# Optimization experiments

Measured on AMD Instinct MI355X. Metric: run time of the kernel, lower is better.

Reference implementation:

```python
import jax, jax.numpy as jnp
import numpy as np

NUM_EXPERTS = 64
TOP_K = 8
TEMPERATURE = 1.0


def setup_inputs() -> dict:
    key = jax.random.key(0)
    k1, k2 = jax.random.split(key)
    B, D, E = 32768, 2048, NUM_EXPERTS
    r = jax.random.normal(k1, (B, D), dtype=jnp.float32)
    W = jax.random.normal(k2, (E, D), dtype=jnp.float32) * (1.0 / np.sqrt(D))
    b = jnp.zeros((E,), dtype=jnp.float32)
    return {"r": r, "W": W, "b": b}


def reference(r, W, b):
    # logits: (B, E) = r @ W^T + b, then temperature scaling
    logits = (jnp.einsum('bd,ed->be', r, W) + b) / TEMPERATURE
    weights_soft = jax.nn.softmax(logits, axis=-1)
    if TOP_K is not None and TOP_K < NUM_EXPERTS:
        topk_vals, topk_idx = jax.lax.top_k(weights_soft, TOP_K)
        mask = jnp.zeros_like(weights_soft)
        mask = jax.vmap(lambda m, i: m.at[i].set(1.0))(mask, topk_idx)
        weights_hard = weights_soft * mask
        weights_hard = weights_hard / (weights_hard.sum(axis=-1, keepdims=True) + 1e-9)
    else:
        weights_hard = weights_soft
    return (weights_hard, weights_soft)
```

## Files before the change

kernel.cpp:

```cpp
#include <hip/hip_runtime.h>
#include <hip/hip_bf16.h>
#include <stdint.h>


#define D_DIM 2048
#define E_DIM 64
#define B_DIM 32768
#define TOPK 8

typedef __bf16 bf16x8 __attribute__((ext_vector_type(8)));
typedef float f32x4 __attribute__((ext_vector_type(4)));

__global__ __launch_bounds__(256) void w_split3(const float* __restrict__ W,
                                                __bf16* __restrict__ W1,
                                                __bf16* __restrict__ W2,
                                                __bf16* __restrict__ W3) {
    int i = (blockIdx.x * 256 + threadIdx.x) * 8;
    bf16x8 o1, o2, o3;
    #pragma unroll
    for (int j = 0; j < 8; ++j) {
        float x  = W[i + j];
        __bf16 h1 = (__bf16)x;
        float r1 = x - (float)h1;
        __bf16 h2 = (__bf16)r1;
        float r2 = r1 - (float)h2;
        o1[j] = h1; o2[j] = h2; o3[j] = (__bf16)r2;
    }
    *(bf16x8*)(W1 + i) = o1;
    *(bf16x8*)(W2 + i) = o2;
    *(bf16x8*)(W3 + i) = o3;
}

__device__ __forceinline__ void gload_lds16(const void* g, void* s) {
    __builtin_amdgcn_global_load_lds(
        (const __attribute__((address_space(1))) unsigned int*)g,
        (__attribute__((address_space(3))) unsigned int*)s,
        16, 0, 0);
}

__global__ __launch_bounds__(256) void moe_gate(const float* __restrict__ r,
                                                const __bf16* __restrict__ W1,
                                                const __bf16* __restrict__ W2,
                                                const __bf16* __restrict__ W3,
                                                const float* __restrict__ bias,
                                                float* __restrict__ out) {
    __shared__ __bf16 bstage[2][3][E_DIM * 32];
    __shared__ float  lg[64][E_DIM + 1];

    const int t    = threadIdx.x;
    const int wv   = t >> 6;
    const int lane = t & 63;
    const int lrow = lane & 15;
    const int quad = lane >> 4;
    const int row0 = blockIdx.x * 64;

    const int se  = t >> 2;
    const int skc = t & 3;
    const size_t sgo = (size_t)se * D_DIM + skc * 8;

    const float* ra = r + (size_t)(row0 + wv * 16 + lrow) * D_DIM + quad * 8;

    f32x4 accM[4] = {};
    f32x4 accD[4] = {};
    f32x4 accL[4] = {};

    gload_lds16(W1 + sgo, &bstage[0][0][t * 8]);
    gload_lds16(W2 + sgo, &bstage[0][1][t * 8]);
    gload_lds16(W3 + sgo, &bstage[0][2][t * 8]);
    float4 a0 = *(const float4*)(ra);
    float4 a1 = *(const float4*)(ra + 4);

    for (int ks = 0; ks < D_DIM / 32; ++ks) {
        __syncthreads();
        const int kn = ks + 1;
        if (kn < D_DIM / 32) {
            const size_t go = sgo + (size_t)kn * 32;
            gload_lds16(W1 + go, &bstage[kn & 1][0][t * 8]);
            gload_lds16(W2 + go, &bstage[kn & 1][1][t * 8]);
            gload_lds16(W3 + go, &bstage[kn & 1][2][t * 8]);
        }

        float av[8] = {a0.x, a0.y, a0.z, a0.w, a1.x, a1.y, a1.z, a1.w};
        if (kn < D_DIM / 32) {
            a0 = *(const float4*)(ra + kn * 32);
            a1 = *(const float4*)(ra + kn * 32 + 4);
        }
        bf16x8 A1, A2, A3;
        #pragma unroll
        for (int j = 0; j < 8; ++j) {
            float x  = av[j];
            __bf16 h1 = (__bf16)x;
            float r1 = x - (float)h1;
            __bf16 h2 = (__bf16)r1;
            float r2 = r1 - (float)h2;
            A1[j] = h1; A2[j] = h2; A3[j] = (__bf16)r2;
        }

        const __bf16* bb = &bstage[ks & 1][0][0];
        const int fo = (quad * 8) + lrow * 32;
        bf16x8 B[3][4];
        #pragma unroll
        for (int s = 0; s < 3; ++s)
            #pragma unroll
            for (int n = 0; n < 4; ++n)
                B[s][n] = *(const bf16x8*)(bb + (size_t)s * E_DIM * 32 + n * 16 * 32 + fo);

        #pragma unroll
        for (int n = 0; n < 4; ++n) {
            accM[n] = __builtin_amdgcn_mfma_f32_16x16x32_bf16(A1, B[0][n], accM[n], 0, 0, 0);
            accD[n] = __builtin_amdgcn_mfma_f32_16x16x32_bf16(A1, B[1][n], accD[n], 0, 0, 0);
            accD[n] = __builtin_amdgcn_mfma_f32_16x16x32_bf16(A2, B[0][n], accD[n], 0, 0, 0);
            accL[n] = __builtin_amdgcn_mfma_f32_16x16x32_bf16(A1, B[2][n], accL[n], 0, 0, 0);
            accL[n] = __builtin_amdgcn_mfma_f32_16x16x32_bf16(A2, B[1][n], accL[n], 0, 0, 0);
            accL[n] = __builtin_amdgcn_mfma_f32_16x16x32_bf16(A3, B[0][n], accL[n], 0, 0, 0);
        }
    }

    #pragma unroll
    for (int n = 0; n < 4; ++n) {
        int col = n * 16 + lrow;
        float bb = bias[col];
        #pragma unroll
        for (int i = 0; i < 4; ++i) {
            lg[wv * 16 + quad * 4 + i][col] = (accM[n][i] + (accD[n][i] + accL[n][i])) + bb;
        }
    }
    __syncthreads();

    for (int rr = wv; rr < 64; rr += 4) {
        float logit = lg[rr][lane];
        float mx = logit;
        #pragma unroll
        for (int s = 32; s >= 1; s >>= 1) mx = fmaxf(mx, __shfl_xor(mx, s));
        float ex = expf(logit - mx);
        float sm = ex;
        #pragma unroll
        for (int s = 32; s >= 1; s >>= 1) sm += __shfl_xor(sm, s);
        float soft = ex / sm;

        bool  sel    = false;
        float topsum = 0.0f;
        #pragma unroll
        for (int it = 0; it < TOPK; ++it) {
            float cand = sel ? -1.0f : soft;
            float cm = cand;
            #pragma unroll
            for (int s = 32; s >= 1; s >>= 1) cm = fmaxf(cm, __shfl_xor(cm, s));
            unsigned long long ball = __ballot(cand == cm);
            int leader = __ffsll(ball) - 1;
            if (lane == leader) sel = true;
            topsum += cm;
        }
        float hard = sel ? soft / (topsum + 1e-9f) : 0.0f;

        size_t orow = (size_t)(row0 + rr) * E_DIM + lane;
        out[orow] = hard;
        out[(size_t)B_DIM * E_DIM + orow] = soft;
    }
}

extern "C" void kernel_launch(void* const* d_in, const int* in_sizes, int n_in,
                              void* d_out, int out_size, void* d_ws, size_t ws_size,
                              hipStream_t stream) {
    const float* r = (const float*)d_in[0];
    const float* W = (const float*)d_in[1];
    const float* b = (const float*)d_in[2];
    float* out = (float*)d_out;
    __bf16* W1 = (__bf16*)d_ws;
    __bf16* W2 = W1 + (size_t)E_DIM * D_DIM;
    __bf16* W3 = W2 + (size_t)E_DIM * D_DIM;

    w_split3<<<64, 256, 0, stream>>>(W, W1, W2, W3);
    moe_gate<<<512, 256, 0, stream>>>(r, W1, W2, W3, b, out);
}
```

Baseline: 433.0 us.

## Split K dimension across two wave groups and pack W chunks contiguously

Each block now runs 512 threads: two halves of four waves each take half of the D dimension for the same 64 rows, and their partial logits are summed through shared memory before the softmax/top-k stage. The weight prep kernel writes the three bf16 splits into a K-chunk-interleaved layout, so each stage load reads one contiguous 12 KB chunk. The shared staging buffer is reused for the logits tile. The aim is more waves in flight per CU to hide r-load latency, at the cost of an extra reduction pass and more barriers.

```diff
diff --git a/kernel.cpp b/kernel.cpp
--- a/kernel.cpp
+++ b/kernel.cpp
@@ -11,24 +11,25 @@
 typedef __bf16 bf16x8 __attribute__((ext_vector_type(8)));
 typedef float f32x4 __attribute__((ext_vector_type(4)));
 
-__global__ __launch_bounds__(256) void w_split3(const float* __restrict__ W,
-                                                __bf16* __restrict__ W1,
-                                                __bf16* __restrict__ W2,
-                                                __bf16* __restrict__ W3) {
-    int i = (blockIdx.x * 256 + threadIdx.x) * 8;
+__global__ __launch_bounds__(256) void w_prep(const float* __restrict__ W,
+                                              __bf16* __restrict__ P) {
+    const int K = blockIdx.x;
+    const int u = threadIdx.x;
+    const float* src = W + (size_t)(u >> 2) * D_DIM + K * 32 + (u & 3) * 8;
+    __bf16* dst = P + (size_t)K * 6144 + u * 8;
     bf16x8 o1, o2, o3;
     #pragma unroll
     for (int j = 0; j < 8; ++j) {
-        float x  = W[i + j];
+        float x  = src[j];
         __bf16 h1 = (__bf16)x;
         float r1 = x - (float)h1;
         __bf16 h2 = (__bf16)r1;
         float r2 = r1 - (float)h2;
         o1[j] = h1; o2[j] = h2; o3[j] = (__bf16)r2;
     }
-    *(bf16x8*)(W1 + i) = o1;
-    *(bf16x8*)(W2 + i) = o2;
-    *(bf16x8*)(W3 + i) = o3;
+    *(bf16x8*)(dst)        = o1;
+    *(bf16x8*)(dst + 2048) = o2;
+    *(bf16x8*)(dst + 4096) = o3;
 }
 
 __device__ __forceinline__ void gload_lds16(const void* g, void* s) {
@@ -38,50 +39,51 @@
         16, 0, 0);
 }
 
-__global__ __launch_bounds__(256) void moe_gate(const float* __restrict__ r,
-                                                const __bf16* __restrict__ W1,
-                                                const __bf16* __restrict__ W2,
-                                                const __bf16* __restrict__ W3,
-                                                const float* __restrict__ bias,
-                                                float* __restrict__ out) {
-    __shared__ __bf16 bstage[2][3][E_DIM * 32];
-    __shared__ float  lg[64][E_DIM + 1];
+__global__ __launch_bounds__(512, 4) void moe_gate(const float* __restrict__ r,
+                                                   const __bf16* __restrict__ P,
+                                                   const float* __restrict__ bias,
+                                                   float* __restrict__ out) {
+    __shared__ __align__(16) char smem[2 * 2 * 3 * 2048 * 2];
+
+    __bf16 (*bstage)[2][3][2048] = reinterpret_cast<__bf16 (*)[2][3][2048]>(smem);
+    float  (*lg)[E_DIM + 1]      = reinterpret_cast<float (*)[E_DIM + 1]>(smem);
 
     const int t    = threadIdx.x;
     const int wv   = t >> 6;
     const int lane = t & 63;
     const int lrow = lane & 15;
     const int quad = lane >> 4;
+    const int h    = wv >> 2;
+    const int wq   = wv & 3;
+    const int tl   = t & 255;
     const int row0 = blockIdx.x * 64;
 
-    const int se  = t >> 2;
-    const int skc = t & 3;
-    const size_t sgo = (size_t)se * D_DIM + skc * 8;
+    const __bf16* Pb = P + (size_t)h * 32 * 6144 + tl * 8;
 
-    const float* ra = r + (size_t)(row0 + wv * 16 + lrow) * D_DIM + quad * 8;
+    const float* ra = r + (size_t)(row0 + wq * 16 + lrow) * D_DIM + h * 1024 + quad * 8;
 
     f32x4 accM[4] = {};
     f32x4 accD[4] = {};
     f32x4 accL[4] = {};
 
-    gload_lds16(W1 + sgo, &bstage[0][0][t * 8]);
-    gload_lds16(W2 + sgo, &bstage[0][1][t * 8]);
-    gload_lds16(W3 + sgo, &bstage[0][2][t * 8]);
+    #pragma unroll
+    for (int s = 0; s < 3; ++s)
+        gload_lds16(Pb + s * 2048, &bstage[h][0][s][tl * 8]);
     float4 a0 = *(const float4*)(ra);
     float4 a1 = *(const float4*)(ra + 4);
 
-    for (int ks = 0; ks < D_DIM / 32; ++ks) {
+    for (int ks = 0; ks < 32; ++ks) {
         __syncthreads();
         const int kn = ks + 1;
-        if (kn < D_DIM / 32) {
-            const size_t go = sgo + (size_t)kn * 32;
-            gload_lds16(W1 + go, &bstage[kn & 1][0][t * 8]);
-            gload_lds16(W2 + go, &bstage[kn & 1][1][t * 8]);
-            gload_lds16(W3 + go, &bstage[kn & 1][2][t * 8]);
+        if (kn < 32) {
+            #pragma unroll
+            for (int s = 0; s < 3; ++s)
+                gload_lds16(Pb + (size_t)kn * 6144 + s * 2048,
+                            &bstage[h][kn & 1][s][tl * 8]);
         }
 
         float av[8] = {a0.x, a0.y, a0.z, a0.w, a1.x, a1.y, a1.z, a1.w};
-        if (kn < D_DIM / 32) {
+        if (kn < 32) {
             a0 = *(const float4*)(ra + kn * 32);
             a1 = *(const float4*)(ra + kn * 32 + 4);
         }
@@ -96,14 +98,14 @@
             A1[j] = h1; A2[j] = h2; A3[j] = (__bf16)r2;
         }
 
-        const __bf16* bb = &bstage[ks & 1][0][0];
-        const int fo = (quad * 8) + lrow * 32;
+        const __bf16* bb = &bstage[h][ks & 1][0][0];
+        const int fo = quad * 8 + lrow * 32;
         bf16x8 B[3][4];
         #pragma unroll
         for (int s = 0; s < 3; ++s)
             #pragma unroll
             for (int n = 0; n < 4; ++n)
-                B[s][n] = *(const bf16x8*)(bb + (size_t)s * E_DIM * 32 + n * 16 * 32 + fo);
+                B[s][n] = *(const bf16x8*)(bb + (size_t)s * 2048 + n * 512 + fo);
 
         #pragma unroll
         for (int n = 0; n < 4; ++n) {
@@ -116,19 +118,32 @@
         }
     }
 
-    #pragma unroll
-    for (int n = 0; n < 4; ++n) {
-        int col = n * 16 + lrow;
-        float bb = bias[col];
+    __syncthreads();
+
+    if (h == 0) {
         #pragma unroll
-        for (int i = 0; i < 4; ++i) {
-            lg[wv * 16 + quad * 4 + i][col] = (accM[n][i] + (accD[n][i] + accL[n][i])) + bb;
+        for (int n = 0; n < 4; ++n) {
+            int col = n * 16 + lrow;
+            #pragma unroll
+            for (int i = 0; i < 4; ++i)
+                lg[wq * 16 + quad * 4 + i][col] = accM[n][i] + (accD[n][i] + accL[n][i]);
+        }
+    }
+    __syncthreads();
+    if (h == 1) {
+        #pragma unroll
+        for (int n = 0; n < 4; ++n) {
+            int col = n * 16 + lrow;
+            #pragma unroll
+            for (int i = 0; i < 4; ++i)
+                lg[wq * 16 + quad * 4 + i][col] += accM[n][i] + (accD[n][i] + accL[n][i]);
         }
     }
     __syncthreads();
 
-    for (int rr = wv; rr < 64; rr += 4) {
-        float logit = lg[rr][lane];
+    const float bcol = bias[lane];
+    for (int rr = wv; rr < 64; rr += 8) {
+        float logit = lg[rr][lane] + bcol;
         float mx = logit;
         #pragma unroll
         for (int s = 32; s >= 1; s >>= 1) mx = fmaxf(mx, __shfl_xor(mx, s));
@@ -166,10 +181,8 @@
     const float* W = (const float*)d_in[1];
     const float* b = (const float*)d_in[2];
     float* out = (float*)d_out;
-    __bf16* W1 = (__bf16*)d_ws;
-    __bf16* W2 = W1 + (size_t)E_DIM * D_DIM;
-    __bf16* W3 = W2 + (size_t)E_DIM * D_DIM;
+    __bf16* P = (__bf16*)d_ws;
 
-    w_split3<<<64, 256, 0, stream>>>(W, W1, W2, W3);
-    moe_gate<<<512, 256, 0, stream>>>(r, W1, W2, W3, b, out);
+    w_prep<<<64, 256, 0, stream>>>(W, P);
+    moe_gate<<<512, 512, 0, stream>>>(r, P, b, out);
 }
```

Result: faster. 412.3 us (-4.8%).
